# Kernel optimization log

Hardware: AMD Instinct MI355X
Metric: run time of the kernel (lower is better)

## Reference

```python
import jax, jax.numpy as jnp
import numpy as np

# --- QTIP TCQ config (matches init_kwargs) ---
M, K = 4096, 4096          # out_features, in_features
TD_X, TD_Y = 16, 16        # tile dims
L = 16                     # trellis state bits
KV = 4                     # bits consumed per step (K=2 bits/weight * V=2)
V = 2                      # weights emitted per step
TLUT_BITS = 9              # lut index bits
T_STEPS = TD_X * TD_Y // V # 128 steps per tile
NBITS = T_STEPS * KV       # 512 bits per tile (tail-biting: exactly K bits/weight)
NWORDS = NBITS // 16       # 32 int16 words per tile
NT = (M // TD_X) * (K // TD_Y)  # 65536 tiles
BATCH, SEQ = 4, 2048


def setup_inputs() -> dict:
    key = jax.random.key(0)
    k1, k2, k3 = jax.random.split(key, 3)
    inp = jax.random.normal(k1, (BATCH, SEQ, K), dtype=jnp.float32)
    # int16 buffer modeled as int32 holding arbitrary 16-bit patterns
    trellis = jax.random.randint(k2, (NT, NWORDS), 0, 65536, dtype=jnp.int32)
    tlut = jax.random.normal(k3, (2 ** TLUT_BITS, V), dtype=jnp.float32) * 0.02
    return {"inp": inp, "trellis": trellis, "tlut": tlut}


def _decode(trellis, tlut):
    """Decode bit-packed tail-biting bitshift trellis codes into dense W [M, K]."""
    words = trellis.astype(jnp.uint32) & 0xFFFF          # uint16 bit patterns
    shifts = (15 - jnp.arange(16)).astype(jnp.uint32)    # MSB-first within word
    bits = ((words[:, :, None] >> shifts) & 1).astype(jnp.int32).reshape(NT, NBITS)
    # step t reads L-bit window starting at t*KV, wrapping around (tail-biting)
    win = (jnp.arange(T_STEPS)[:, None] * KV + jnp.arange(L)[None, :]) % NBITS  # [T, L]
    bw = bits[:, win]                                    # [NT, T, L]
    pow2 = (2 ** (L - 1 - jnp.arange(L))).astype(jnp.int32)
    state = jnp.einsum('ntl,l->nt', bw, pow2)            # L-bit state per step
    code = state & (2 ** TLUT_BITS - 1)                  # low tlut_bits index the lut
    w = tlut[code].reshape(NT, TD_X, TD_Y)               # V outputs/step, row-major tile
    # tiles are laid out row-major over (M//td_x, K//td_y)
    w = w.reshape(M // TD_X, K // TD_Y, TD_X, TD_Y).transpose(0, 2, 1, 3).reshape(M, K)
    return w


def reference(inp, trellis, tlut):
    Wd = _decode(trellis, tlut)          # [M, K]
    x = inp.reshape(-1, K)               # [bs, K]
    y = x @ Wd.T                         # [bs, M]
    return y.reshape(*inp.shape[:-1], M).astype(inp.dtype)
```

## Files before the change

kernel.cpp:

```cpp
#include <hip/hip_runtime.h>
#include <hip/hip_bf16.h>

#define AS1 __attribute__((address_space(1)))
#define AS3 __attribute__((address_space(3)))

typedef __bf16 bf16x8 __attribute__((ext_vector_type(8)));
typedef float f32x4 __attribute__((ext_vector_type(4)));

#define GLOAD_LDS16(gptr, lptr) \
  __builtin_amdgcn_global_load_lds((AS1 void*)(gptr), (AS3 void*)(lptr), 16, 0, 0)

#define M_W   4096
#define K_DIM 4096
#define M_X   8192
#define NT_T  65536
#define TSTEPS 128
#define NKT   (K_DIM/64)

#define BAR()        __builtin_amdgcn_s_barrier()
#define WAIT_LGKM0() asm volatile("s_waitcnt lgkmcnt(0)" ::: "memory")
#define WAIT_LGKM8() asm volatile("s_waitcnt lgkmcnt(8)" ::: "memory")
#define WAIT_VM4()   asm volatile("s_waitcnt vmcnt(4)" ::: "memory")
#define WAIT_VM0()   asm volatile("s_waitcnt vmcnt(0)" ::: "memory")

__device__ __forceinline__ unsigned short f2bf(float f) {
  unsigned int u = __float_as_uint(f);
  unsigned int r = (u + 0x7FFFu + ((u >> 16) & 1u)) >> 16;
  return (unsigned short)r;
}

__global__ void cvt_kernel(const float* __restrict__ x, unsigned short* __restrict__ xb) {
  int idx = blockIdx.x * blockDim.x + threadIdx.x;
  const float4* p = reinterpret_cast<const float4*>(x) + (size_t)idx * 2;
  float4 u = p[0];
  float4 v = p[1];
  uint4 o;
  o.x = (unsigned)f2bf(u.x) | ((unsigned)f2bf(u.y) << 16);
  o.y = (unsigned)f2bf(u.z) | ((unsigned)f2bf(u.w) << 16);
  o.z = (unsigned)f2bf(v.x) | ((unsigned)f2bf(v.y) << 16);
  o.w = (unsigned)f2bf(v.z) | ((unsigned)f2bf(v.w) << 16);
  reinterpret_cast<uint4*>(xb)[idx] = o;
}

__global__ void decode_kernel(const int* __restrict__ trellis,
                              const float* __restrict__ tlut,
                              unsigned short* __restrict__ W) {
  int idx = blockIdx.x * blockDim.x + threadIdx.x;
  int t = idx >> 7;
  int s = idx & 127;
  const unsigned int* tr = reinterpret_cast<const unsigned int*>(trellis) + t * 32;
  int w0  = s >> 2;
  int off = (s & 3) * 4;
  unsigned int a = tr[w0] & 0xFFFFu;
  unsigned int state;
  if (off == 0) {
    state = a;
  } else {
    unsigned int b = tr[(w0 + 1) & 31] & 0xFFFFu;
    state = ((a << off) | (b >> (16 - off))) & 0xFFFFu;
  }
  unsigned int code = state & 0x1FFu;
  float2 v = reinterpret_cast<const float2*>(tlut)[code];
  int i = t >> 8;
  int j = t & 255;
  int flat = s * 2;
  int r = flat >> 4;
  int c = flat & 15;
  unsigned int packed = (unsigned)f2bf(v.x) | ((unsigned)f2bf(v.y) << 16);
  size_t o = (size_t)(i * 16 + r) * K_DIM + (j * 16 + c);
  *reinterpret_cast<unsigned int*>(W + o) = packed;
}


template<int BUF, int MH>
__device__ __forceinline__ void lda(const char* ldsc, const int* aRow, const int* kOff,
                                    bf16x8 af[4][2]) {
  const char* base = ldsc + (BUF * 2 + MH) * 16384;
  #pragma unroll
  for (int fm = 0; fm < 4; ++fm)
    #pragma unroll
    for (int kh = 0; kh < 2; ++kh)
      af[fm][kh] = *(const bf16x8*)(base + aRow[fm] + kOff[kh]);
}

template<int BUF, int NH>
__device__ __forceinline__ void ldb(const char* ldsc, const int* bRow, const int* kOff,
                                    bf16x8 bq[2][2]) {
  const char* base = ldsc + 65536 + (BUF * 2 + NH) * 16384;
  #pragma unroll
  for (int fn = 0; fn < 2; ++fn)
    #pragma unroll
    for (int kh = 0; kh < 2; ++kh)
      bq[fn][kh] = *(const bf16x8*)(base + bRow[fn] + kOff[kh]);
}

template<int MH, int NH>
__device__ __forceinline__ void mm(bf16x8 af[4][2], bf16x8 bq[2][2], f32x4 acc[8][4]) {
  __builtin_amdgcn_s_setprio(1);
  #pragma unroll
  for (int fm = 0; fm < 4; ++fm)
    #pragma unroll
    for (int fn = 0; fn < 2; ++fn)
      #pragma unroll
      for (int kh = 0; kh < 2; ++kh)
        acc[MH * 4 + fm][NH * 2 + fn] =
            __builtin_amdgcn_mfma_f32_16x16x32_bf16(af[fm][kh], bq[fn][kh],
                                                    acc[MH * 4 + fm][NH * 2 + fn], 0, 0, 0);
  __builtin_amdgcn_s_setprio(0);
}

template<int BUF, int HALF>
__device__ __forceinline__ void stA(const unsigned short* xb, char* ldsc, int kt,
                                    int gArow0, int gArow1, int gcol, int lo0, int lo1) {
  const unsigned short* s0 = xb + (size_t)(gArow0 + HALF * 64) * K_DIM + kt * 64 + gcol;
  const unsigned short* s1 = xb + (size_t)(gArow1 + HALF * 64) * K_DIM + kt * 64 + gcol;
  GLOAD_LDS16(s0, ldsc + (BUF * 2 + HALF) * 16384 + lo0);
  GLOAD_LDS16(s1, ldsc + (BUF * 2 + HALF) * 16384 + lo1);
}

template<int BUF, int HALF>
__device__ __forceinline__ void stB(const unsigned short* W, char* ldsc, int kt,
                                    int gBrow0, int gBrow1, int gcol, int lo0, int lo1) {
  const unsigned short* s0 = W + (size_t)(gBrow0 + HALF * 32) * K_DIM + kt * 64 + gcol;
  const unsigned short* s1 = W + (size_t)(gBrow1 + HALF * 32) * K_DIM + kt * 64 + gcol;
  GLOAD_LDS16(s0, ldsc + 65536 + (BUF * 2 + HALF) * 16384 + lo0);
  GLOAD_LDS16(s1, ldsc + 65536 + (BUF * 2 + HALF) * 16384 + lo1);
}

__global__ __launch_bounds__(512) void gemm8_kernel(const unsigned short* __restrict__ xb,
                                                    const unsigned short* __restrict__ W,
                                                    float* __restrict__ y) {
  extern __shared__ __align__(16) char ldsc[];

  int bid = blockIdx.x;
  int swz = (bid & 7) * 64 + (bid >> 3);
  int brow = (swz >> 4) * 256;
  int bcol = (swz & 15) * 256;

  int tid  = threadIdx.x;
  int lane = tid & 63;
  int wid  = tid >> 6;
  int wr = wid >> 2;
  int wc = wid & 3;

  int kOff[2], aRow[4], bRow[2];
  #pragma unroll
  for (int kh = 0; kh < 2; ++kh) kOff[kh] = ((kh * 4 + (lane >> 4)) ^ (lane & 7)) << 4;
  #pragma unroll
  for (int fm = 0; fm < 4; ++fm) aRow[fm] = (wr * 64 + fm * 16 + (lane & 15)) << 7;
  #pragma unroll
  for (int fn = 0; fn < 2; ++fn) bRow[fn] = (wc * 32 + fn * 16 + (lane & 15)) << 7;

  int q0 = wid * 16 + (lane >> 3);
  int q1 = q0 + 8;
  int lo0 = wid * 2048 + lane * 16;
  int lo1 = lo0 + 1024;
  int gcol = ((lane & 7) ^ (lane >> 3)) << 3;
  int gArow0 = brow + (q0 >> 6) * 128 + (q0 & 63);
  int gArow1 = brow + (q1 >> 6) * 128 + (q1 & 63);
  int gBrow0 = bcol + (q0 >> 5) * 64 + (q0 & 31);
  int gBrow1 = bcol + (q1 >> 5) * 64 + (q1 & 31);

  f32x4 acc[8][4];
  #pragma unroll
  for (int m = 0; m < 8; ++m)
    #pragma unroll
    for (int n = 0; n < 4; ++n)
      acc[m][n] = (f32x4){0.f, 0.f, 0.f, 0.f};

  bf16x8 af[4][2];
  bf16x8 bq[2][2][2];

  stA<0,0>(xb, ldsc, 0, gArow0, gArow1, gcol, lo0, lo1);
  stB<0,1>(W,  ldsc, 0, gBrow0, gBrow1, gcol, lo0, lo1);
  stA<0,1>(xb, ldsc, 0, gArow0, gArow1, gcol, lo0, lo1);
  stB<0,0>(W,  ldsc, 0, gBrow0, gBrow1, gcol, lo0, lo1);
  stA<1,0>(xb, ldsc, 1, gArow0, gArow1, gcol, lo0, lo1);
  stB<1,1>(W,  ldsc, 1, gBrow0, gBrow1, gcol, lo0, lo1);
  WAIT_VM4(); BAR();

  #pragma unroll 1
  for (int i = 0; i < NKT / 2; ++i) {
    int t1 = 2 * i + 1;
    int t2 = 2 * i + 2; if (t2 > NKT - 1) t2 = NKT - 1;
    int t3 = 2 * i + 3; if (t3 > NKT - 1) t3 = NKT - 1;

    lda<0,0>(ldsc, aRow, kOff, af);
    ldb<0,0>(ldsc, bRow, kOff, bq[0]);
    stA<1,1>(xb, ldsc, t1, gArow0, gArow1, gcol, lo0, lo1);
    WAIT_LGKM8(); BAR(); WAIT_LGKM0();
    mm<0,0>(af, bq[0], acc);
    BAR();
    ldb<0,1>(ldsc, bRow, kOff, bq[1]);
    stB<1,0>(W, ldsc, t1, gBrow0, gBrow1, gcol, lo0, lo1);
    BAR(); WAIT_LGKM0();
    mm<0,1>(af, bq[1], acc);
    BAR();
    lda<0,1>(ldsc, aRow, kOff, af);
    stA<0,0>(xb, ldsc, t2, gArow0, gArow1, gcol, lo0, lo1);
    BAR(); WAIT_LGKM0();
    mm<1,1>(af, bq[1], acc);
    BAR();
    stB<0,1>(W, ldsc, t2, gBrow0, gBrow1, gcol, lo0, lo1);
    WAIT_VM4(); BAR();
    mm<1,0>(af, bq[0], acc);
    BAR();
    lda<1,0>(ldsc, aRow, kOff, af);
    ldb<1,0>(ldsc, bRow, kOff, bq[0]);
    stA<0,1>(xb, ldsc, t2, gArow0, gArow1, gcol, lo0, lo1);
    WAIT_LGKM8(); BAR(); WAIT_LGKM0();
    mm<0,0>(af, bq[0], acc);
    BAR();
    ldb<1,1>(ldsc, bRow, kOff, bq[1]);
    stB<0,0>(W, ldsc, t2, gBrow0, gBrow1, gcol, lo0, lo1);
    BAR(); WAIT_LGKM0();
    mm<0,1>(af, bq[1], acc);
    BAR();
    lda<1,1>(ldsc, aRow, kOff, af);
    stA<1,0>(xb, ldsc, t3, gArow0, gArow1, gcol, lo0, lo1);
    BAR(); WAIT_LGKM0();
    mm<1,1>(af, bq[1], acc);
    BAR();
    stB<1,1>(W, ldsc, t3, gBrow0, gBrow1, gcol, lo0, lo1);
    WAIT_VM4(); BAR();
    mm<1,0>(af, bq[0], acc);
    BAR();
  }

  WAIT_VM0(); BAR();

  #pragma unroll
  for (int am = 0; am < 8; ++am) {
    #pragma unroll
    for (int an = 0; an < 4; ++an) {
      int row0 = brow + wr * 128 + am * 16 + (lane >> 4) * 4;
      int col  = bcol + wc * 64 + an * 16 + (lane & 15);
      #pragma unroll
      for (int j = 0; j < 4; ++j)
        y[(size_t)(row0 + j) * M_W + col] = acc[am][an][j];
    }
  }
}

extern "C" void kernel_launch(void* const* d_in, const int* in_sizes, int n_in,
                              void* d_out, int out_size, void* d_ws, size_t ws_size,
                              hipStream_t stream) {
  const float* inp     = (const float*)d_in[0];
  const int*   trellis = (const int*)d_in[1];
  const float* tlut    = (const float*)d_in[2];
  float* y = (float*)d_out;

  unsigned short* xb = (unsigned short*)d_ws;
  unsigned short* Wd = (unsigned short*)((char*)d_ws + (size_t)M_X * K_DIM * 2);

  (void)hipFuncSetAttribute((const void*)gemm8_kernel,
                            hipFuncAttributeMaxDynamicSharedMemorySize, 131072);

  cvt_kernel<<<M_X * K_DIM / 8 / 256, 256, 0, stream>>>(inp, xb);
  decode_kernel<<<NT_T * TSTEPS / 256, 256, 0, stream>>>(trellis, tlut, Wd);
  gemm8_kernel<<<dim3(512), dim3(512), 131072, stream>>>(xb, Wd, y);
}
```

Measured before the change: 280.1 us.

## Restructure GEMM main loop into register double-buffered 8-phase pipeline

Rewrites the bf16 GEMM main loop so LDS fragment reads for the next quarter-tile go into a second register set while the current MFMAs run. Explicit lgkmcnt waits are dropped, and phases are separated by sched_barrier, vmcnt(6) and a single barrier each, which halves the barriers per phase. It also reorders the MFMA loop (kh outermost), precomputes LDS addresses, and sets launch_bounds to 2 blocks per CU. The aim is to hide LDS latency and cut synchronisation stalls, at the cost of more VGPRs for the doubled fragments. The relaxed wait discipline relies on the compiler's implicit LDS waits and on the store/read ordering of the pipeline staying correct.

```diff
diff --git a/kernel.cpp b/kernel.cpp
--- a/kernel.cpp
+++ b/kernel.cpp
@@ -17,11 +17,10 @@
 #define TSTEPS 128
 #define NKT   (K_DIM/64)
 
-#define BAR()        __builtin_amdgcn_s_barrier()
-#define WAIT_LGKM0() asm volatile("s_waitcnt lgkmcnt(0)" ::: "memory")
-#define WAIT_LGKM8() asm volatile("s_waitcnt lgkmcnt(8)" ::: "memory")
-#define WAIT_VM4()   asm volatile("s_waitcnt vmcnt(4)" ::: "memory")
-#define WAIT_VM0()   asm volatile("s_waitcnt vmcnt(0)" ::: "memory")
+#define BAR()    __builtin_amdgcn_s_barrier()
+#define SCHED0() __builtin_amdgcn_sched_barrier(0)
+#define VM6()    asm volatile("s_waitcnt vmcnt(6)" ::: "memory")
+#define VM0()    asm volatile("s_waitcnt vmcnt(0)" ::: "memory")
 
 __device__ __forceinline__ unsigned short f2bf(float f) {
   unsigned int u = __float_as_uint(f);
@@ -72,37 +71,34 @@
 }
 
 
-template<int BUF, int MH>
-__device__ __forceinline__ void lda(const char* ldsc, const int* aRow, const int* kOff,
-                                    bf16x8 af[4][2]) {
-  const char* base = ldsc + (BUF * 2 + MH) * 16384;
-  #pragma unroll
-  for (int fm = 0; fm < 4; ++fm)
+template<int SB>
+__device__ __forceinline__ void lda2(const char* ldsc, int a0, int a1, bf16x8 af[4][2]) {
+  #pragma unroll
+  for (int fm = 0; fm < 4; ++fm) {
+    af[fm][0] = *(const bf16x8*)(ldsc + SB + fm * 2048 + a0);
+    af[fm][1] = *(const bf16x8*)(ldsc + SB + fm * 2048 + a1);
+  }
+}
+
+template<int SB>
+__device__ __forceinline__ void ldb2(const char* ldsc, int b0, int b1, bf16x8 bq[2][2]) {
+  #pragma unroll
+  for (int fn = 0; fn < 2; ++fn) {
+    bq[fn][0] = *(const bf16x8*)(ldsc + SB + fn * 2048 + b0);
+    bq[fn][1] = *(const bf16x8*)(ldsc + SB + fn * 2048 + b1);
+  }
+}
+
+template<int MH, int NH>
+__device__ __forceinline__ void mmq(const bf16x8 af[4][2], const bf16x8 bq[2][2],
+                                    f32x4 acc[8][4]) {
+  __builtin_amdgcn_s_setprio(1);
+  #pragma unroll
+  for (int kh = 0; kh < 2; ++kh)
     #pragma unroll
-    for (int kh = 0; kh < 2; ++kh)
-      af[fm][kh] = *(const bf16x8*)(base + aRow[fm] + kOff[kh]);
-}
-
-template<int BUF, int NH>
-__device__ __forceinline__ void ldb(const char* ldsc, const int* bRow, const int* kOff,
-                                    bf16x8 bq[2][2]) {
-  const char* base = ldsc + 65536 + (BUF * 2 + NH) * 16384;
-  #pragma unroll
-  for (int fn = 0; fn < 2; ++fn)
-    #pragma unroll
-    for (int kh = 0; kh < 2; ++kh)
-      bq[fn][kh] = *(const bf16x8*)(base + bRow[fn] + kOff[kh]);
-}
-
-template<int MH, int NH>
-__device__ __forceinline__ void mm(bf16x8 af[4][2], bf16x8 bq[2][2], f32x4 acc[8][4]) {
-  __builtin_amdgcn_s_setprio(1);
-  #pragma unroll
-  for (int fm = 0; fm < 4; ++fm)
-    #pragma unroll
-    for (int fn = 0; fn < 2; ++fn)
+    for (int fm = 0; fm < 4; ++fm)
       #pragma unroll
-      for (int kh = 0; kh < 2; ++kh)
+      for (int fn = 0; fn < 2; ++fn)
         acc[MH * 4 + fm][NH * 2 + fn] =
             __builtin_amdgcn_mfma_f32_16x16x32_bf16(af[fm][kh], bq[fn][kh],
                                                     acc[MH * 4 + fm][NH * 2 + fn], 0, 0, 0);
@@ -111,25 +107,25 @@
 
 template<int BUF, int HALF>
 __device__ __forceinline__ void stA(const unsigned short* xb, char* ldsc, int kt,
-                                    int gArow0, int gArow1, int gcol, int lo0, int lo1) {
+                                    int gArow0, int gArow1, int gcol, int lo0) {
   const unsigned short* s0 = xb + (size_t)(gArow0 + HALF * 64) * K_DIM + kt * 64 + gcol;
   const unsigned short* s1 = xb + (size_t)(gArow1 + HALF * 64) * K_DIM + kt * 64 + gcol;
   GLOAD_LDS16(s0, ldsc + (BUF * 2 + HALF) * 16384 + lo0);
-  GLOAD_LDS16(s1, ldsc + (BUF * 2 + HALF) * 16384 + lo1);
+  GLOAD_LDS16(s1, ldsc + (BUF * 2 + HALF) * 16384 + lo0 + 1024);
 }
 
 template<int BUF, int HALF>
 __device__ __forceinline__ void stB(const unsigned short* W, char* ldsc, int kt,
-                                    int gBrow0, int gBrow1, int gcol, int lo0, int lo1) {
+                                    int gBrow0, int gBrow1, int gcol, int lo0) {
   const unsigned short* s0 = W + (size_t)(gBrow0 + HALF * 32) * K_DIM + kt * 64 + gcol;
   const unsigned short* s1 = W + (size_t)(gBrow1 + HALF * 32) * K_DIM + kt * 64 + gcol;
   GLOAD_LDS16(s0, ldsc + 65536 + (BUF * 2 + HALF) * 16384 + lo0);
-  GLOAD_LDS16(s1, ldsc + 65536 + (BUF * 2 + HALF) * 16384 + lo1);
-}
-
-__global__ __launch_bounds__(512) void gemm8_kernel(const unsigned short* __restrict__ xb,
-                                                    const unsigned short* __restrict__ W,
-                                                    float* __restrict__ y) {
+  GLOAD_LDS16(s1, ldsc + 65536 + (BUF * 2 + HALF) * 16384 + lo0 + 1024);
+}
+
+__global__ __launch_bounds__(512, 2) void gemm8_kernel(const unsigned short* __restrict__ xb,
+                                                       const unsigned short* __restrict__ W,
+                                                       float* __restrict__ y) {
   extern __shared__ __align__(16) char ldsc[];
 
   int bid = blockIdx.x;
@@ -143,18 +139,17 @@
   int wr = wid >> 2;
   int wc = wid & 3;
 
-  int kOff[2], aRow[4], bRow[2];
-  #pragma unroll
-  for (int kh = 0; kh < 2; ++kh) kOff[kh] = ((kh * 4 + (lane >> 4)) ^ (lane & 7)) << 4;
-  #pragma unroll
-  for (int fm = 0; fm < 4; ++fm) aRow[fm] = (wr * 64 + fm * 16 + (lane & 15)) << 7;
-  #pragma unroll
-  for (int fn = 0; fn < 2; ++fn) bRow[fn] = (wc * 32 + fn * 16 + (lane & 15)) << 7;
+  int lr = lane >> 4, la7 = lane & 7, lc = lane & 15;
+  int k0 = (lr ^ la7) << 4;
+  int k1 = ((4 + lr) ^ la7) << 4;
+  int a0 = (wr * 64 + lc) * 128 + k0;
+  int a1 = (wr * 64 + lc) * 128 + k1;
+  int b0 = (wc * 32 + lc) * 128 + k0;
+  int b1 = (wc * 32 + lc) * 128 + k1;
 
   int q0 = wid * 16 + (lane >> 3);
   int q1 = q0 + 8;
   int lo0 = wid * 2048 + lane * 16;
-  int lo1 = lo0 + 1024;
   int gcol = ((lane & 7) ^ (lane >> 3)) << 3;
   int gArow0 = brow + (q0 >> 6) * 128 + (q0 & 63);
   int gArow1 = brow + (q1 >> 6) * 128 + (q1 & 63);
@@ -168,16 +163,20 @@
     for (int n = 0; n < 4; ++n)
       acc[m][n] = (f32x4){0.f, 0.f, 0.f, 0.f};
 
-  bf16x8 af[4][2];
-  bf16x8 bq[2][2][2];
-
-  stA<0,0>(xb, ldsc, 0, gArow0, gArow1, gcol, lo0, lo1);
-  stB<0,1>(W,  ldsc, 0, gBrow0, gBrow1, gcol, lo0, lo1);
-  stA<0,1>(xb, ldsc, 0, gArow0, gArow1, gcol, lo0, lo1);
-  stB<0,0>(W,  ldsc, 0, gBrow0, gBrow1, gcol, lo0, lo1);
-  stA<1,0>(xb, ldsc, 1, gArow0, gArow1, gcol, lo0, lo1);
-  stB<1,1>(W,  ldsc, 1, gBrow0, gBrow1, gcol, lo0, lo1);
-  WAIT_VM4(); BAR();
+  bf16x8 afA[4][2], afB[4][2];
+  bf16x8 bqX[2][2], bqY[2][2];
+
+  stA<0,0>(xb, ldsc, 0, gArow0, gArow1, gcol, lo0);
+  stB<0,0>(W,  ldsc, 0, gBrow0, gBrow1, gcol, lo0);
+  stB<0,1>(W,  ldsc, 0, gBrow0, gBrow1, gcol, lo0);
+  stA<0,1>(xb, ldsc, 0, gArow0, gArow1, gcol, lo0);
+  stA<1,0>(xb, ldsc, 1, gArow0, gArow1, gcol, lo0);
+  stB<1,0>(W,  ldsc, 1, gBrow0, gBrow1, gcol, lo0);
+  stB<1,1>(W,  ldsc, 1, gBrow0, gBrow1, gcol, lo0);
+  VM0(); BAR();
+
+  lda2<0 * 16384>(ldsc, a0, a1, afA);
+  ldb2<65536 + 0 * 16384>(ldsc, b0, b1, bqX);
 
   #pragma unroll 1
   for (int i = 0; i < NKT / 2; ++i) {
@@ -185,49 +184,56 @@
     int t2 = 2 * i + 2; if (t2 > NKT - 1) t2 = NKT - 1;
     int t3 = 2 * i + 3; if (t3 > NKT - 1) t3 = NKT - 1;
 
-    lda<0,0>(ldsc, aRow, kOff, af);
-    ldb<0,0>(ldsc, bRow, kOff, bq[0]);
-    stA<1,1>(xb, ldsc, t1, gArow0, gArow1, gcol, lo0, lo1);
-    WAIT_LGKM8(); BAR(); WAIT_LGKM0();
-    mm<0,0>(af, bq[0], acc);
-    BAR();
-    ldb<0,1>(ldsc, bRow, kOff, bq[1]);
-    stB<1,0>(W, ldsc, t1, gBrow0, gBrow1, gcol, lo0, lo1);
-    BAR(); WAIT_LGKM0();
-    mm<0,1>(af, bq[1], acc);
-    BAR();
-    lda<0,1>(ldsc, aRow, kOff, af);
-    stA<0,0>(xb, ldsc, t2, gArow0, gArow1, gcol, lo0, lo1);
-    BAR(); WAIT_LGKM0();
-    mm<1,1>(af, bq[1], acc);
-    BAR();
-    stB<0,1>(W, ldsc, t2, gBrow0, gBrow1, gcol, lo0, lo1);
-    WAIT_VM4(); BAR();
-    mm<1,0>(af, bq[0], acc);
-    BAR();
-    lda<1,0>(ldsc, aRow, kOff, af);
-    ldb<1,0>(ldsc, bRow, kOff, bq[0]);
-    stA<0,1>(xb, ldsc, t2, gArow0, gArow1, gcol, lo0, lo1);
-    WAIT_LGKM8(); BAR(); WAIT_LGKM0();
-    mm<0,0>(af, bq[0], acc);
-    BAR();
-    ldb<1,1>(ldsc, bRow, kOff, bq[1]);
-    stB<0,0>(W, ldsc, t2, gBrow0, gBrow1, gcol, lo0, lo1);
-    BAR(); WAIT_LGKM0();
-    mm<0,1>(af, bq[1], acc);
-    BAR();
-    lda<1,1>(ldsc, aRow, kOff, af);
-    stA<1,0>(xb, ldsc, t3, gArow0, gArow1, gcol, lo0, lo1);
-    BAR(); WAIT_LGKM0();
-    mm<1,1>(af, bq[1], acc);
-    BAR();
-    stB<1,1>(W, ldsc, t3, gBrow0, gBrow1, gcol, lo0, lo1);
-    WAIT_VM4(); BAR();
-    mm<1,0>(af, bq[0], acc);
-    BAR();
-  }
-
-  WAIT_VM0(); BAR();
+    lda2<1 * 16384>(ldsc, a0, a1, afB);
+    stA<1,1>(xb, ldsc, t1, gArow0, gArow1, gcol, lo0);
+    SCHED0();
+    mmq<0,0>(afA, bqX, acc);
+    VM6(); BAR();
+
+    ldb2<65536 + 1 * 16384>(ldsc, b0, b1, bqY);
+    stA<0,0>(xb, ldsc, t2, gArow0, gArow1, gcol, lo0);
+    SCHED0();
+    mmq<1,0>(afB, bqX, acc);
+    VM6(); BAR();
+
+    stB<0,0>(W, ldsc, t2, gBrow0, gBrow1, gcol, lo0);
+    SCHED0();
+    mmq<1,1>(afB, bqY, acc);
+    VM6(); BAR();
+
+    lda2<2 * 16384>(ldsc, a0, a1, afB);
+    ldb2<65536 + 2 * 16384>(ldsc, b0, b1, bqX);
+    stB<0,1>(W, ldsc, t2, gBrow0, gBrow1, gcol, lo0);
+    SCHED0();
+    mmq<0,1>(afA, bqY, acc);
+    VM6(); BAR();
+
+    lda2<3 * 16384>(ldsc, a0, a1, afA);
+    stA<0,1>(xb, ldsc, t2, gArow0, gArow1, gcol, lo0);
+    SCHED0();
+    mmq<0,0>(afB, bqX, acc);
+    VM6(); BAR();
+
+    ldb2<65536 + 3 * 16384>(ldsc, b0, b1, bqY);
+    stA<1,0>(xb, ldsc, t3, gArow0, gArow1, gcol, lo0);
+    SCHED0();
+    mmq<1,0>(afA, bqX, acc);
+    VM6(); BAR();
+
+    stB<1,0>(W, ldsc, t3, gBrow0, gBrow1, gcol, lo0);
+    SCHED0();
+    mmq<1,1>(afA, bqY, acc);
+    VM6(); BAR();
+
+    lda2<0 * 16384>(ldsc, a0, a1, afA);
+    ldb2<65536 + 0 * 16384>(ldsc, b0, b1, bqX);
+    stB<1,1>(W, ldsc, t3, gBrow0, gBrow1, gcol, lo0);
+    SCHED0();
+    mmq<0,1>(afB, bqY, acc);
+    VM6(); BAR();
+  }
+
+  VM0();
 
   #pragma unroll
   for (int am = 0; am < 8; ++am) {
```

Measured after the change: 283.9 us. Within noise of the previous version (+1.4%).

## Fuse prep kernels and restructure GEMM k-loop with ping-pong wave parity

Applied to the files above, without the earlier changes.

Merges the fp32-to-bf16 activation conversion and the trellis decode into a single interleaved prep launch. The GEMM main loop is rewritten into eight phases with double-buffered A/B fragment registers, one barrier per phase, and two wave groups that alternate between issuing LDS reads and running MFMA, so each group's matrix math overlaps the other's loads. The intent is to cut barrier stalls and launch overhead, at the cost of more live registers and subtle waitcnt correctness risk.

```diff
diff --git a/kernel.cpp b/kernel.cpp
--- a/kernel.cpp
+++ b/kernel.cpp
@@ -14,14 +14,19 @@
 #define K_DIM 4096
 #define M_X   8192
 #define NT_T  65536
-#define TSTEPS 128
 #define NKT   (K_DIM/64)
 
-#define BAR()        __builtin_amdgcn_s_barrier()
-#define WAIT_LGKM0() asm volatile("s_waitcnt lgkmcnt(0)" ::: "memory")
-#define WAIT_LGKM8() asm volatile("s_waitcnt lgkmcnt(8)" ::: "memory")
-#define WAIT_VM4()   asm volatile("s_waitcnt vmcnt(4)" ::: "memory")
-#define WAIT_VM0()   asm volatile("s_waitcnt vmcnt(0)" ::: "memory")
+#define BAR()    __builtin_amdgcn_s_barrier()
+#define SCHED0() __builtin_amdgcn_sched_barrier(0)
+#define VMW6()   asm volatile("s_waitcnt vmcnt(6)" ::: "memory")
+#define VMW0()   asm volatile("s_waitcnt vmcnt(0)" ::: "memory")
+
+template<int N> __device__ __forceinline__ void lgkmw() {
+  if constexpr (N == 0)       asm volatile("s_waitcnt lgkmcnt(0)" ::: "memory");
+  else if constexpr (N == 4)  asm volatile("s_waitcnt lgkmcnt(4)" ::: "memory");
+  else if constexpr (N == 8)  asm volatile("s_waitcnt lgkmcnt(8)" ::: "memory");
+  else                        asm volatile("s_waitcnt lgkmcnt(12)" ::: "memory");
+}
 
 __device__ __forceinline__ unsigned short f2bf(float f) {
   unsigned int u = __float_as_uint(f);
@@ -29,52 +34,57 @@
   return (unsigned short)r;
 }
 
-__global__ void cvt_kernel(const float* __restrict__ x, unsigned short* __restrict__ xb) {
-  int idx = blockIdx.x * blockDim.x + threadIdx.x;
-  const float4* p = reinterpret_cast<const float4*>(x) + (size_t)idx * 2;
-  float4 u = p[0];
-  float4 v = p[1];
-  uint4 o;
-  o.x = (unsigned)f2bf(u.x) | ((unsigned)f2bf(u.y) << 16);
-  o.y = (unsigned)f2bf(u.z) | ((unsigned)f2bf(u.w) << 16);
-  o.z = (unsigned)f2bf(v.x) | ((unsigned)f2bf(v.y) << 16);
-  o.w = (unsigned)f2bf(v.z) | ((unsigned)f2bf(v.w) << 16);
-  reinterpret_cast<uint4*>(xb)[idx] = o;
-}
-
-__global__ void decode_kernel(const int* __restrict__ trellis,
-                              const float* __restrict__ tlut,
-                              unsigned short* __restrict__ W) {
-  int idx = blockIdx.x * blockDim.x + threadIdx.x;
-  int t = idx >> 7;
-  int s = idx & 127;
-  const unsigned int* tr = reinterpret_cast<const unsigned int*>(trellis) + t * 32;
-  int w0  = s >> 2;
-  int off = (s & 3) * 4;
-  unsigned int a = tr[w0] & 0xFFFFu;
-  unsigned int state;
-  if (off == 0) {
-    state = a;
+__global__ void prep_kernel(const float* __restrict__ x,
+                            const int* __restrict__ trellis,
+                            const float* __restrict__ tlut,
+                            unsigned short* __restrict__ xb,
+                            unsigned short* __restrict__ W) {
+  int b = blockIdx.x;
+  int tid = threadIdx.x;
+  if (b % 3 == 0) {
+    int idx = (b / 3) * 256 + tid;
+    const float4* p = reinterpret_cast<const float4*>(x) + (size_t)idx * 2;
+    float4 u = p[0];
+    float4 v = p[1];
+    uint4 o;
+    o.x = (unsigned)f2bf(u.x) | ((unsigned)f2bf(u.y) << 16);
+    o.y = (unsigned)f2bf(u.z) | ((unsigned)f2bf(u.w) << 16);
+    o.z = (unsigned)f2bf(v.x) | ((unsigned)f2bf(v.y) << 16);
+    o.w = (unsigned)f2bf(v.z) | ((unsigned)f2bf(v.w) << 16);
+    reinterpret_cast<uint4*>(xb)[idx] = o;
   } else {
-    unsigned int b = tr[(w0 + 1) & 31] & 0xFFFFu;
-    state = ((a << off) | (b >> (16 - off))) & 0xFFFFu;
+    int db = b - b / 3 - 1;
+    int idx = db * 256 + tid;
+    int t = idx >> 7;
+    int s = idx & 127;
+    const unsigned int* tr = reinterpret_cast<const unsigned int*>(trellis) + t * 32;
+    int w0  = s >> 2;
+    int off = (s & 3) * 4;
+    unsigned int a = tr[w0] & 0xFFFFu;
+    unsigned int state;
+    if (off == 0) {
+      state = a;
+    } else {
+      unsigned int bb = tr[(w0 + 1) & 31] & 0xFFFFu;
+      state = ((a << off) | (bb >> (16 - off))) & 0xFFFFu;
+    }
+    unsigned int code = state & 0x1FFu;
+    float2 v = reinterpret_cast<const float2*>(tlut)[code];
+    int i = t >> 8;
+    int j = t & 255;
+    int flat = s * 2;
+    int r = flat >> 4;
+    int c = flat & 15;
+    unsigned int packed = (unsigned)f2bf(v.x) | ((unsigned)f2bf(v.y) << 16);
+    size_t o = (size_t)(i * 16 + r) * K_DIM + (j * 16 + c);
+    *reinterpret_cast<unsigned int*>(W + o) = packed;
   }
-  unsigned int code = state & 0x1FFu;
-  float2 v = reinterpret_cast<const float2*>(tlut)[code];
-  int i = t >> 8;
-  int j = t & 255;
-  int flat = s * 2;
-  int r = flat >> 4;
-  int c = flat & 15;
-  unsigned int packed = (unsigned)f2bf(v.x) | ((unsigned)f2bf(v.y) << 16);
-  size_t o = (size_t)(i * 16 + r) * K_DIM + (j * 16 + c);
-  *reinterpret_cast<unsigned int*>(W + o) = packed;
 }
 
 
 template<int BUF, int MH>
 __device__ __forceinline__ void lda(const char* ldsc, const int* aRow, const int* kOff,
-                                    bf16x8 af[4][2]) {
+                                    bf16x8 (&af)[4][2]) {
   const char* base = ldsc + (BUF * 2 + MH) * 16384;
   #pragma unroll
   for (int fm = 0; fm < 4; ++fm)
@@ -85,7 +95,7 @@
 
 template<int BUF, int NH>
 __device__ __forceinline__ void ldb(const char* ldsc, const int* bRow, const int* kOff,
-                                    bf16x8 bq[2][2]) {
+                                    bf16x8 (&bq)[2][2]) {
   const char* base = ldsc + 65536 + (BUF * 2 + NH) * 16384;
   #pragma unroll
   for (int fn = 0; fn < 2; ++fn)
@@ -95,7 +105,8 @@
 }
 
 template<int MH, int NH>
-__device__ __forceinline__ void mm(bf16x8 af[4][2], bf16x8 bq[2][2], f32x4 acc[8][4]) {
+__device__ __forceinline__ void mm(const bf16x8 (&af)[4][2], const bf16x8 (&bq)[2][2],
+                                   f32x4 (&acc)[8][4]) {
   __builtin_amdgcn_s_setprio(1);
   #pragma unroll
   for (int fm = 0; fm < 4; ++fm)
@@ -111,20 +122,71 @@
 
 template<int BUF, int HALF>
 __device__ __forceinline__ void stA(const unsigned short* xb, char* ldsc, int kt,
-                                    int gArow0, int gArow1, int gcol, int lo0, int lo1) {
+                                    int gArow0, int gArow1, int gcol, int lo0) {
   const unsigned short* s0 = xb + (size_t)(gArow0 + HALF * 64) * K_DIM + kt * 64 + gcol;
   const unsigned short* s1 = xb + (size_t)(gArow1 + HALF * 64) * K_DIM + kt * 64 + gcol;
   GLOAD_LDS16(s0, ldsc + (BUF * 2 + HALF) * 16384 + lo0);
-  GLOAD_LDS16(s1, ldsc + (BUF * 2 + HALF) * 16384 + lo1);
+  GLOAD_LDS16(s1, ldsc + (BUF * 2 + HALF) * 16384 + lo0 + 1024);
 }
 
 template<int BUF, int HALF>
 __device__ __forceinline__ void stB(const unsigned short* W, char* ldsc, int kt,
-                                    int gBrow0, int gBrow1, int gcol, int lo0, int lo1) {
+                                    int gBrow0, int gBrow1, int gcol, int lo0) {
   const unsigned short* s0 = W + (size_t)(gBrow0 + HALF * 32) * K_DIM + kt * 64 + gcol;
   const unsigned short* s1 = W + (size_t)(gBrow1 + HALF * 32) * K_DIM + kt * 64 + gcol;
   GLOAD_LDS16(s0, ldsc + 65536 + (BUF * 2 + HALF) * 16384 + lo0);
-  GLOAD_LDS16(s1, ldsc + 65536 + (BUF * 2 + HALF) * 16384 + lo1);
+  GLOAD_LDS16(s1, ldsc + 65536 + (BUF * 2 + HALF) * 16384 + lo0 + 1024);
+}
+
+#define PHASE(RD, ST, LG, MMCALL)                         \
+  if (PA) {                                               \
+    RD; ST; SCHED0(); lgkmw<LG>(); SCHED0();              \
+    MMCALL;                                               \
+  } else {                                                \
+    lgkmw<0>(); SCHED0();                                 \
+    MMCALL;                                               \
+    SCHED0(); RD; ST;                                     \
+  }                                                       \
+  VMW6(); BAR();
+
+template<bool PA>
+__device__ __forceinline__ void kloop(const unsigned short* __restrict__ xb,
+                                      const unsigned short* __restrict__ W,
+                                      char* ldsc, const int* aRow, const int* bRow,
+                                      const int* kOff, int gArow0, int gArow1,
+                                      int gBrow0, int gBrow1, int gcol, int lo0,
+                                      bf16x8 (&afA)[4][2], bf16x8 (&afB)[4][2],
+                                      bf16x8 (&bqX)[2][2], bf16x8 (&bqY)[2][2],
+                                      f32x4 (&acc)[8][4]) {
+  #pragma unroll 1
+  for (int i = 0; i < NKT / 2; ++i) {
+    int t1 = 2 * i + 1;
+    int t2 = 2 * i + 2; if (t2 > NKT - 1) t2 = NKT - 1;
+    int t3 = 2 * i + 3; if (t3 > NKT - 1) t3 = NKT - 1;
+
+    PHASE((lda<0,1>(ldsc, aRow, kOff, afB)),
+          (stA<1,1>(xb, ldsc, t1, gArow0, gArow1, gcol, lo0)), 8,
+          (mm<0,0>(afA, bqX, acc)));
+    PHASE((ldb<0,1>(ldsc, bRow, kOff, bqY)),
+          (stA<0,0>(xb, ldsc, t2, gArow0, gArow1, gcol, lo0)), 4,
+          (mm<1,0>(afB, bqX, acc)));
+    PHASE(, (stB<0,0>(W, ldsc, t2, gBrow0, gBrow1, gcol, lo0)), 0,
+          (mm<1,1>(afB, bqY, acc)));
+    PHASE((lda<1,0>(ldsc, aRow, kOff, afB), ldb<1,0>(ldsc, bRow, kOff, bqX)),
+          (stB<0,1>(W, ldsc, t2, gBrow0, gBrow1, gcol, lo0)), 12,
+          (mm<0,1>(afA, bqY, acc)));
+    PHASE((lda<1,1>(ldsc, aRow, kOff, afA)),
+          (stA<0,1>(xb, ldsc, t2, gArow0, gArow1, gcol, lo0)), 8,
+          (mm<0,0>(afB, bqX, acc)));
+    PHASE((ldb<1,1>(ldsc, bRow, kOff, bqY)),
+          (stA<1,0>(xb, ldsc, t3, gArow0, gArow1, gcol, lo0)), 4,
+          (mm<1,0>(afA, bqX, acc)));
+    PHASE(, (stB<1,0>(W, ldsc, t3, gBrow0, gBrow1, gcol, lo0)), 0,
+          (mm<1,1>(afA, bqY, acc)));
+    PHASE((lda<0,0>(ldsc, aRow, kOff, afA), ldb<0,0>(ldsc, bRow, kOff, bqX)),
+          (stB<1,1>(W, ldsc, t3, gBrow0, gBrow1, gcol, lo0)), 12,
+          (mm<0,1>(afB, bqY, acc)));
+  }
 }
 
 __global__ __launch_bounds__(512) void gemm8_kernel(const unsigned short* __restrict__ xb,
@@ -142,6 +204,7 @@
   int wid  = tid >> 6;
   int wr = wid >> 2;
   int wc = wid & 3;
+  bool parA = ((wid ^ (wid >> 2)) & 1) == 0;
 
   int kOff[2], aRow[4], bRow[2];
   #pragma unroll
@@ -154,7 +217,6 @@
   int q0 = wid * 16 + (lane >> 3);
   int q1 = q0 + 8;
   int lo0 = wid * 2048 + lane * 16;
-  int lo1 = lo0 + 1024;
   int gcol = ((lane & 7) ^ (lane >> 3)) << 3;
   int gArow0 = brow + (q0 >> 6) * 128 + (q0 & 63);
   int gArow1 = brow + (q1 >> 6) * 128 + (q1 & 63);
@@ -168,66 +230,29 @@
     for (int n = 0; n < 4; ++n)
       acc[m][n] = (f32x4){0.f, 0.f, 0.f, 0.f};
 
-  bf16x8 af[4][2];
-  bf16x8 bq[2][2][2];
-
-  stA<0,0>(xb, ldsc, 0, gArow0, gArow1, gcol, lo0, lo1);
-  stB<0,1>(W,  ldsc, 0, gBrow0, gBrow1, gcol, lo0, lo1);
-  stA<0,1>(xb, ldsc, 0, gArow0, gArow1, gcol, lo0, lo1);
-  stB<0,0>(W,  ldsc, 0, gBrow0, gBrow1, gcol, lo0, lo1);
-  stA<1,0>(xb, ldsc, 1, gArow0, gArow1, gcol, lo0, lo1);
-  stB<1,1>(W,  ldsc, 1, gBrow0, gBrow1, gcol, lo0, lo1);
-  WAIT_VM4(); BAR();
-
-  #pragma unroll 1
-  for (int i = 0; i < NKT / 2; ++i) {
-    int t1 = 2 * i + 1;
-    int t2 = 2 * i + 2; if (t2 > NKT - 1) t2 = NKT - 1;
-    int t3 = 2 * i + 3; if (t3 > NKT - 1) t3 = NKT - 1;
-
-    lda<0,0>(ldsc, aRow, kOff, af);
-    ldb<0,0>(ldsc, bRow, kOff, bq[0]);
-    stA<1,1>(xb, ldsc, t1, gArow0, gArow1, gcol, lo0, lo1);
-    WAIT_LGKM8(); BAR(); WAIT_LGKM0();
-    mm<0,0>(af, bq[0], acc);
-    BAR();
-    ldb<0,1>(ldsc, bRow, kOff, bq[1]);
-    stB<1,0>(W, ldsc, t1, gBrow0, gBrow1, gcol, lo0, lo1);
-    BAR(); WAIT_LGKM0();
-    mm<0,1>(af, bq[1], acc);
-    BAR();
-    lda<0,1>(ldsc, aRow, kOff, af);
-    stA<0,0>(xb, ldsc, t2, gArow0, gArow1, gcol, lo0, lo1);
-    BAR(); WAIT_LGKM0();
-    mm<1,1>(af, bq[1], acc);
-    BAR();
-    stB<0,1>(W, ldsc, t2, gBrow0, gBrow1, gcol, lo0, lo1);
-    WAIT_VM4(); BAR();
-    mm<1,0>(af, bq[0], acc);
-    BAR();
-    lda<1,0>(ldsc, aRow, kOff, af);
-    ldb<1,0>(ldsc, bRow, kOff, bq[0]);
-    stA<0,1>(xb, ldsc, t2, gArow0, gArow1, gcol, lo0, lo1);
-    WAIT_LGKM8(); BAR(); WAIT_LGKM0();
-    mm<0,0>(af, bq[0], acc);
-    BAR();
-    ldb<1,1>(ldsc, bRow, kOff, bq[1]);
-    stB<0,0>(W, ldsc, t2, gBrow0, gBrow1, gcol, lo0, lo1);
-    BAR(); WAIT_LGKM0();
-    mm<0,1>(af, bq[1], acc);
-    BAR();
-    lda<1,1>(ldsc, aRow, kOff, af);
-    stA<1,0>(xb, ldsc, t3, gArow0, gArow1, gcol, lo0, lo1);
-    BAR(); WAIT_LGKM0();
-    mm<1,1>(af, bq[1], acc);
-    BAR();
-    stB<1,1>(W, ldsc, t3, gBrow0, gBrow1, gcol, lo0, lo1);
-    WAIT_VM4(); BAR();
-    mm<1,0>(af, bq[0], acc);
-    BAR();
-  }
-
-  WAIT_VM0(); BAR();
+  bf16x8 afA[4][2], afB[4][2];
+  bf16x8 bqX[2][2], bqY[2][2];
+
+  stA<0,0>(xb, ldsc, 0, gArow0, gArow1, gcol, lo0);
+  stB<0,0>(W,  ldsc, 0, gBrow0, gBrow1, gcol, lo0);
+  stB<0,1>(W,  ldsc, 0, gBrow0, gBrow1, gcol, lo0);
+  stA<0,1>(xb, ldsc, 0, gArow0, gArow1, gcol, lo0);
+  stA<1,0>(xb, ldsc, 1, gArow0, gArow1, gcol, lo0);
+  stB<1,0>(W,  ldsc, 1, gBrow0, gBrow1, gcol, lo0);
+  stB<1,1>(W,  ldsc, 1, gBrow0, gBrow1, gcol, lo0);
+  VMW0(); BAR();
+
+  lda<0,0>(ldsc, aRow, kOff, afA);
+  ldb<0,0>(ldsc, bRow, kOff, bqX);
+
+  if (parA)
+    kloop<true>(xb, W, ldsc, aRow, bRow, kOff, gArow0, gArow1, gBrow0, gBrow1,
+                gcol, lo0, afA, afB, bqX, bqY, acc);
+  else
+    kloop<false>(xb, W, ldsc, aRow, bRow, kOff, gArow0, gArow1, gBrow0, gBrow1,
+                 gcol, lo0, afA, afB, bqX, bqY, acc);
+
+  VMW0();
 
   #pragma unroll
   for (int am = 0; am < 8; ++am) {
@@ -256,7 +281,6 @@
   (void)hipFuncSetAttribute((const void*)gemm8_kernel,
                             hipFuncAttributeMaxDynamicSharedMemorySize, 131072);
 
-  cvt_kernel<<<M_X * K_DIM / 8 / 256, 256, 0, stream>>>(inp, xb);
-  decode_kernel<<<NT_T * TSTEPS / 256, 256, 0, stream>>>(trellis, tlut, Wd);
+  prep_kernel<<<49152, 256, 0, stream>>>(inp, trellis, tlut, xb, Wd);
   gemm8_kernel<<<dim3(512), dim3(512), 131072, stream>>>(xb, Wd, y);
 }
```

Measured after the change: 297.9 us. +6.3%, slower.

## Fuse cvt and decode into one prep kernel and restructure GEMM pipeline into four phases

Applied to the files above, without the earlier changes.

Merges the activation bf16 conversion and trellis decode into a single launch, with blocks interleaved 1:2 between the two jobs to save a launch and its tail. In the GEMM main loop, each k-tile is now handled by loading both B halves at once and running the two MFMA groups back-to-back. This halves the number of barrier-separated phases and reorders the global->LDS prefetches. The risks are higher register pressure from holding both B fragments and a changed overlap of loads with compute under the new waitcnt placement.

```diff
diff --git a/kernel.cpp b/kernel.cpp
--- a/kernel.cpp
+++ b/kernel.cpp
@@ -14,7 +14,6 @@
 #define K_DIM 4096
 #define M_X   8192
 #define NT_T  65536
-#define TSTEPS 128
 #define NKT   (K_DIM/64)
 
 #define BAR()        __builtin_amdgcn_s_barrier()
@@ -29,52 +28,57 @@
   return (unsigned short)r;
 }
 
-__global__ void cvt_kernel(const float* __restrict__ x, unsigned short* __restrict__ xb) {
-  int idx = blockIdx.x * blockDim.x + threadIdx.x;
-  const float4* p = reinterpret_cast<const float4*>(x) + (size_t)idx * 2;
-  float4 u = p[0];
-  float4 v = p[1];
-  uint4 o;
-  o.x = (unsigned)f2bf(u.x) | ((unsigned)f2bf(u.y) << 16);
-  o.y = (unsigned)f2bf(u.z) | ((unsigned)f2bf(u.w) << 16);
-  o.z = (unsigned)f2bf(v.x) | ((unsigned)f2bf(v.y) << 16);
-  o.w = (unsigned)f2bf(v.z) | ((unsigned)f2bf(v.w) << 16);
-  reinterpret_cast<uint4*>(xb)[idx] = o;
-}
-
-__global__ void decode_kernel(const int* __restrict__ trellis,
-                              const float* __restrict__ tlut,
-                              unsigned short* __restrict__ W) {
-  int idx = blockIdx.x * blockDim.x + threadIdx.x;
-  int t = idx >> 7;
-  int s = idx & 127;
-  const unsigned int* tr = reinterpret_cast<const unsigned int*>(trellis) + t * 32;
-  int w0  = s >> 2;
-  int off = (s & 3) * 4;
-  unsigned int a = tr[w0] & 0xFFFFu;
-  unsigned int state;
-  if (off == 0) {
-    state = a;
+__global__ void prep_kernel(const float* __restrict__ x,
+                            const int* __restrict__ trellis,
+                            const float* __restrict__ tlut,
+                            unsigned short* __restrict__ xb,
+                            unsigned short* __restrict__ W) {
+  int b = blockIdx.x;
+  int tid = threadIdx.x;
+  if (b % 3 == 0) {
+    int idx = (b / 3) * 256 + tid;
+    const float4* p = reinterpret_cast<const float4*>(x) + (size_t)idx * 2;
+    float4 u = p[0];
+    float4 v = p[1];
+    uint4 o;
+    o.x = (unsigned)f2bf(u.x) | ((unsigned)f2bf(u.y) << 16);
+    o.y = (unsigned)f2bf(u.z) | ((unsigned)f2bf(u.w) << 16);
+    o.z = (unsigned)f2bf(v.x) | ((unsigned)f2bf(v.y) << 16);
+    o.w = (unsigned)f2bf(v.z) | ((unsigned)f2bf(v.w) << 16);
+    reinterpret_cast<uint4*>(xb)[idx] = o;
   } else {
-    unsigned int b = tr[(w0 + 1) & 31] & 0xFFFFu;
-    state = ((a << off) | (b >> (16 - off))) & 0xFFFFu;
+    int db = b - b / 3 - 1;
+    int idx = db * 256 + tid;
+    int t = idx >> 7;
+    int s = idx & 127;
+    const unsigned int* tr = reinterpret_cast<const unsigned int*>(trellis) + t * 32;
+    int w0  = s >> 2;
+    int off = (s & 3) * 4;
+    unsigned int a = tr[w0] & 0xFFFFu;
+    unsigned int state;
+    if (off == 0) {
+      state = a;
+    } else {
+      unsigned int bb = tr[(w0 + 1) & 31] & 0xFFFFu;
+      state = ((a << off) | (bb >> (16 - off))) & 0xFFFFu;
+    }
+    unsigned int code = state & 0x1FFu;
+    float2 v = reinterpret_cast<const float2*>(tlut)[code];
+    int i = t >> 8;
+    int j = t & 255;
+    int flat = s * 2;
+    int r = flat >> 4;
+    int c = flat & 15;
+    unsigned int packed = (unsigned)f2bf(v.x) | ((unsigned)f2bf(v.y) << 16);
+    size_t o = (size_t)(i * 16 + r) * K_DIM + (j * 16 + c);
+    *reinterpret_cast<unsigned int*>(W + o) = packed;
   }
-  unsigned int code = state & 0x1FFu;
-  float2 v = reinterpret_cast<const float2*>(tlut)[code];
-  int i = t >> 8;
-  int j = t & 255;
-  int flat = s * 2;
-  int r = flat >> 4;
-  int c = flat & 15;
-  unsigned int packed = (unsigned)f2bf(v.x) | ((unsigned)f2bf(v.y) << 16);
-  size_t o = (size_t)(i * 16 + r) * K_DIM + (j * 16 + c);
-  *reinterpret_cast<unsigned int*>(W + o) = packed;
 }
 
 
 template<int BUF, int MH>
 __device__ __forceinline__ void lda(const char* ldsc, const int* aRow, const int* kOff,
-                                    bf16x8 af[4][2]) {
+                                    bf16x8 (&af)[4][2]) {
   const char* base = ldsc + (BUF * 2 + MH) * 16384;
   #pragma unroll
   for (int fm = 0; fm < 4; ++fm)
@@ -85,7 +89,7 @@
 
 template<int BUF, int NH>
 __device__ __forceinline__ void ldb(const char* ldsc, const int* bRow, const int* kOff,
-                                    bf16x8 bq[2][2]) {
+                                    bf16x8 (&bq)[2][2]) {
   const char* base = ldsc + 65536 + (BUF * 2 + NH) * 16384;
   #pragma unroll
   for (int fn = 0; fn < 2; ++fn)
@@ -95,8 +99,8 @@
 }
 
 template<int MH, int NH>
-__device__ __forceinline__ void mm(bf16x8 af[4][2], bf16x8 bq[2][2], f32x4 acc[8][4]) {
-  __builtin_amdgcn_s_setprio(1);
+__device__ __forceinline__ void mm(const bf16x8 (&af)[4][2], const bf16x8 (&bq)[2][2],
+                                   f32x4 (&acc)[8][4]) {
   #pragma unroll
   for (int fm = 0; fm < 4; ++fm)
     #pragma unroll
@@ -106,25 +110,24 @@
         acc[MH * 4 + fm][NH * 2 + fn] =
             __builtin_amdgcn_mfma_f32_16x16x32_bf16(af[fm][kh], bq[fn][kh],
                                                     acc[MH * 4 + fm][NH * 2 + fn], 0, 0, 0);
-  __builtin_amdgcn_s_setprio(0);
 }
 
 template<int BUF, int HALF>
 __device__ __forceinline__ void stA(const unsigned short* xb, char* ldsc, int kt,
-                                    int gArow0, int gArow1, int gcol, int lo0, int lo1) {
+                                    int gArow0, int gArow1, int gcol, int lo0) {
   const unsigned short* s0 = xb + (size_t)(gArow0 + HALF * 64) * K_DIM + kt * 64 + gcol;
   const unsigned short* s1 = xb + (size_t)(gArow1 + HALF * 64) * K_DIM + kt * 64 + gcol;
   GLOAD_LDS16(s0, ldsc + (BUF * 2 + HALF) * 16384 + lo0);
-  GLOAD_LDS16(s1, ldsc + (BUF * 2 + HALF) * 16384 + lo1);
+  GLOAD_LDS16(s1, ldsc + (BUF * 2 + HALF) * 16384 + lo0 + 1024);
 }
 
 template<int BUF, int HALF>
 __device__ __forceinline__ void stB(const unsigned short* W, char* ldsc, int kt,
-                                    int gBrow0, int gBrow1, int gcol, int lo0, int lo1) {
+                                    int gBrow0, int gBrow1, int gcol, int lo0) {
   const unsigned short* s0 = W + (size_t)(gBrow0 + HALF * 32) * K_DIM + kt * 64 + gcol;
   const unsigned short* s1 = W + (size_t)(gBrow1 + HALF * 32) * K_DIM + kt * 64 + gcol;
   GLOAD_LDS16(s0, ldsc + 65536 + (BUF * 2 + HALF) * 16384 + lo0);
-  GLOAD_LDS16(s1, ldsc + 65536 + (BUF * 2 + HALF) * 16384 + lo1);
+  GLOAD_LDS16(s1, ldsc + 65536 + (BUF * 2 + HALF) * 16384 + lo0 + 1024);
 }
 
 __global__ __launch_bounds__(512) void gemm8_kernel(const unsigned short* __restrict__ xb,
@@ -154,7 +157,6 @@
   int q0 = wid * 16 + (lane >> 3);
   int q1 = q0 + 8;
   int lo0 = wid * 2048 + lane * 16;
-  int lo1 = lo0 + 1024;
   int gcol = ((lane & 7) ^ (lane >> 3)) << 3;
   int gArow0 = brow + (q0 >> 6) * 128 + (q0 & 63);
   int gArow1 = brow + (q1 >> 6) * 128 + (q1 & 63);
@@ -169,15 +171,15 @@
       acc[m][n] = (f32x4){0.f, 0.f, 0.f, 0.f};
 
   bf16x8 af[4][2];
-  bf16x8 bq[2][2][2];
-
-  stA<0,0>(xb, ldsc, 0, gArow0, gArow1, gcol, lo0, lo1);
-  stB<0,1>(W,  ldsc, 0, gBrow0, gBrow1, gcol, lo0, lo1);
-  stA<0,1>(xb, ldsc, 0, gArow0, gArow1, gcol, lo0, lo1);
-  stB<0,0>(W,  ldsc, 0, gBrow0, gBrow1, gcol, lo0, lo1);
-  stA<1,0>(xb, ldsc, 1, gArow0, gArow1, gcol, lo0, lo1);
-  stB<1,1>(W,  ldsc, 1, gBrow0, gBrow1, gcol, lo0, lo1);
-  WAIT_VM4(); BAR();
+  bf16x8 bq0[2][2], bq1[2][2];
+
+  stA<0,0>(xb, ldsc, 0, gArow0, gArow1, gcol, lo0);
+  stB<0,0>(W,  ldsc, 0, gBrow0, gBrow1, gcol, lo0);
+  stB<0,1>(W,  ldsc, 0, gBrow0, gBrow1, gcol, lo0);
+  stA<0,1>(xb, ldsc, 0, gArow0, gArow1, gcol, lo0);
+  stA<1,0>(xb, ldsc, 1, gArow0, gArow1, gcol, lo0);
+  stB<1,0>(W,  ldsc, 1, gBrow0, gBrow1, gcol, lo0);
+  WAIT_VM0(); BAR();
 
   #pragma unroll 1
   for (int i = 0; i < NKT / 2; ++i) {
@@ -186,45 +188,48 @@
     int t3 = 2 * i + 3; if (t3 > NKT - 1) t3 = NKT - 1;
 
     lda<0,0>(ldsc, aRow, kOff, af);
-    ldb<0,0>(ldsc, bRow, kOff, bq[0]);
-    stA<1,1>(xb, ldsc, t1, gArow0, gArow1, gcol, lo0, lo1);
+    ldb<0,0>(ldsc, bRow, kOff, bq0);
+    ldb<0,1>(ldsc, bRow, kOff, bq1);
+    stB<1,1>(W,  ldsc, t1, gBrow0, gBrow1, gcol, lo0);
+    stA<1,1>(xb, ldsc, t1, gArow0, gArow1, gcol, lo0);
     WAIT_LGKM8(); BAR(); WAIT_LGKM0();
-    mm<0,0>(af, bq[0], acc);
-    BAR();
-    ldb<0,1>(ldsc, bRow, kOff, bq[1]);
-    stB<1,0>(W, ldsc, t1, gBrow0, gBrow1, gcol, lo0, lo1);
+    __builtin_amdgcn_s_setprio(1);
+    mm<0,0>(af, bq0, acc);
+    mm<0,1>(af, bq1, acc);
+    __builtin_amdgcn_s_setprio(0);
+    WAIT_VM4(); BAR();
+
+    lda<0,1>(ldsc, aRow, kOff, af);
+    stA<0,0>(xb, ldsc, t2, gArow0, gArow1, gcol, lo0);
+    stB<0,0>(W,  ldsc, t2, gBrow0, gBrow1, gcol, lo0);
     BAR(); WAIT_LGKM0();
-    mm<0,1>(af, bq[1], acc);
-    BAR();
-    lda<0,1>(ldsc, aRow, kOff, af);
-    stA<0,0>(xb, ldsc, t2, gArow0, gArow1, gcol, lo0, lo1);
+    __builtin_amdgcn_s_setprio(1);
+    mm<1,0>(af, bq0, acc);
+    mm<1,1>(af, bq1, acc);
+    __builtin_amdgcn_s_setprio(0);
+    WAIT_VM4(); BAR();
+
+    lda<1,0>(ldsc, aRow, kOff, af);
+    ldb<1,0>(ldsc, bRow, kOff, bq0);
+    ldb<1,1>(ldsc, bRow, kOff, bq1);
+    stB<0,1>(W,  ldsc, t2, gBrow0, gBrow1, gcol, lo0);
+    stA<0,1>(xb, ldsc, t2, gArow0, gArow1, gcol, lo0);
+    WAIT_LGKM8(); BAR(); WAIT_LGKM0();
+    __builtin_amdgcn_s_setprio(1);
+    mm<0,0>(af, bq0, acc);
+    mm<0,1>(af, bq1, acc);
+    __builtin_amdgcn_s_setprio(0);
+    WAIT_VM4(); BAR();
+
+    lda<1,1>(ldsc, aRow, kOff, af);
+    stA<1,0>(xb, ldsc, t3, gArow0, gArow1, gcol, lo0);
+    stB<1,0>(W,  ldsc, t3, gBrow0, gBrow1, gcol, lo0);
     BAR(); WAIT_LGKM0();
-    mm<1,1>(af, bq[1], acc);
-    BAR();
-    stB<0,1>(W, ldsc, t2, gBrow0, gBrow1, gcol, lo0, lo1);
-    WAIT_VM4(); BAR();
-    mm<1,0>(af, bq[0], acc);
-    BAR();
-    lda<1,0>(ldsc, aRow, kOff, af);
-    ldb<1,0>(ldsc, bRow, kOff, bq[0]);
-    stA<0,1>(xb, ldsc, t2, gArow0, gArow1, gcol, lo0, lo1);
-    WAIT_LGKM8(); BAR(); WAIT_LGKM0();
-    mm<0,0>(af, bq[0], acc);
-    BAR();
-    ldb<1,1>(ldsc, bRow, kOff, bq[1]);
-    stB<0,0>(W, ldsc, t2, gBrow0, gBrow1, gcol, lo0, lo1);
-    BAR(); WAIT_LGKM0();
-    mm<0,1>(af, bq[1], acc);
-    BAR();
-    lda<1,1>(ldsc, aRow, kOff, af);
-    stA<1,0>(xb, ldsc, t3, gArow0, gArow1, gcol, lo0, lo1);
-    BAR(); WAIT_LGKM0();
-    mm<1,1>(af, bq[1], acc);
-    BAR();
-    stB<1,1>(W, ldsc, t3, gBrow0, gBrow1, gcol, lo0, lo1);
-    WAIT_VM4(); BAR();
-    mm<1,0>(af, bq[0], acc);
-    BAR();
+    __builtin_amdgcn_s_setprio(1);
+    mm<1,0>(af, bq0, acc);
+    mm<1,1>(af, bq1, acc);
+    __builtin_amdgcn_s_setprio(0);
+    WAIT_VM4(); BAR();
   }
 
   WAIT_VM0(); BAR();
@@ -256,7 +261,6 @@
   (void)hipFuncSetAttribute((const void*)gemm8_kernel,
                             hipFuncAttributeMaxDynamicSharedMemorySize, 131072);
 
-  cvt_kernel<<<M_X * K_DIM / 8 / 256, 256, 0, stream>>>(inp, xb);
-  decode_kernel<<<NT_T * TSTEPS / 256, 256, 0, stream>>>(trellis, tlut, Wd);
+  prep_kernel<<<49152, 256, 0, stream>>>(inp, trellis, tlut, xb, Wd);
   gemm8_kernel<<<dim3(512), dim3(512), 131072, stream>>>(xb, Wd, y);
 }
```

Result: faster. 269.8 us (-3.7%).
